# Optimization experiments

Hardware: AMD Instinct MI355X
Metric: run time of the kernel (lower is better)

Reference implementation:

```python
import jax, jax.numpy as jnp
import numpy as np

N = 100000
E = 1600000
DIMS = [256, 192, 128, 64, 3]  # in_features=256, hidden_layer_count=4, last layer -> 3


def setup_inputs() -> dict:
    key = jax.random.key(0)
    ks = jax.random.split(key, 2 + 4 * len(DIMS))
    features = jax.random.normal(ks[0], (N, 256), dtype=jnp.float32)
    # (torch.unique-based normalization implicitly assumes this)
    src = jnp.arange(E, dtype=jnp.int64) % N
    dst = jax.random.randint(ks[1], (E,), 0, N, dtype=jnp.int64)
    edges = jnp.stack([src, dst], axis=1)
    inp = {"features": features, "edges": edges}
    ki = 2
    for li in range(4):
        din, dout = DIMS[li], DIMS[li + 1]
        s = 1.0 / np.sqrt(din)
        inp[f"W0_{li}"] = jax.random.uniform(ks[ki], (din, dout), jnp.float32, -s, s); ki += 1
        inp[f"b0_{li}"] = jax.random.uniform(ks[ki], (dout,), jnp.float32, -s, s); ki += 1
        inp[f"W1_{li}"] = jax.random.uniform(ks[ki], (din, dout), jnp.float32, -s, s); ki += 1
        inp[f"b1_{li}"] = jax.random.uniform(ks[ki], (dout,), jnp.float32, -s, s); ki += 1
    return inp


def _graph_conv_norm(x, edges, deg_inv, W0, b0, W1, b1):
    # pytorch3d GraphConv (undirected): w0(x) + scatter-add of w1(x[neighbor]) over both edge directions,
    # then degree normalization (GraphConvNorm)
    h0 = x @ W0 + b0                       # [N, dout]
    h1 = x @ W1 + b1                       # [N, dout]
    agg = jnp.zeros_like(h0)
    agg = agg.at[edges[:, 0]].add(h1[edges[:, 1]])
    agg = agg.at[edges[:, 1]].add(h1[edges[:, 0]])
    return deg_inv * (h0 + agg)


def reference(features, edges, W0_0, b0_0, W1_0, b1_0, W0_1, b0_1, W1_1, b1_1,
              W0_2, b0_2, W1_2, b1_2, W0_3, b0_3, W1_3, b1_3):
    # degree = occurrence count of each vertex id in edges (== torch.unique(..., return_counts=True)[1])
    deg = jnp.zeros((N,), jnp.float32).at[edges.reshape(-1)].add(1.0)
    deg_inv = (1.0 / deg)[:, None]
    params = [(W0_0, b0_0, W1_0, b1_0), (W0_1, b0_1, W1_1, b1_1), (W0_2, b0_2, W1_2, b1_2)]
    x = features
    for (W0, b0, W1, b1) in params:
        x = jax.nn.relu(_graph_conv_norm(x, edges, deg_inv, W0, b0, W1, b1))
    return _graph_conv_norm(x, edges, deg_inv, W0_3, b0_3, W1_3, b1_3)
```

## Files before the change

kernel.cpp:

```cpp
#include <hip/hip_runtime.h>
#include <hip/hip_fp16.h>

#define NV 100000
#define NE 1600000

#define BM 64
#define BN 64
#define BK 16

#define TBM 128
#define TBN 64
#define TBK 32
#define APAD 40
#define BPAD 40

#define SCAN_B 1024
#define NBLK ((NV + SCAN_B - 1) / SCAN_B)

typedef __attribute__((ext_vector_type(8))) _Float16 f16x8;
typedef __attribute__((ext_vector_type(4))) _Float16 f16x4;
typedef __attribute__((ext_vector_type(2))) _Float16 f16x2;
typedef __attribute__((ext_vector_type(4))) float f32x4;

__global__ void degree_count(const int* __restrict__ ef, int* __restrict__ deg, int n) {
    int i = blockIdx.x * blockDim.x + threadIdx.x;
    if (i < n) atomicAdd(&deg[ef[i]], 1);
}

__global__ __launch_bounds__(SCAN_B) void scan_block(const int* __restrict__ deg,
                                                     int* __restrict__ part,
                                                     int* __restrict__ bsum, int n) {
    __shared__ int tmp[SCAN_B];
    const int tid = threadIdx.x;
    const int gid = blockIdx.x * SCAN_B + tid;
    int v = (gid < n) ? deg[gid] : 0;
    tmp[tid] = v;
    __syncthreads();
    for (int off = 1; off < SCAN_B; off <<= 1) {
        int t = (tid >= off) ? tmp[tid - off] : 0;
        __syncthreads();
        tmp[tid] += t;
        __syncthreads();
    }
    if (gid < n) part[gid] = tmp[tid] - v;
    if (tid == SCAN_B - 1) bsum[blockIdx.x] = tmp[tid];
}

__global__ __launch_bounds__(128) void scan_top(int* __restrict__ bsum, int nb) {
    __shared__ int tmp[128];
    const int tid = threadIdx.x;
    int v = (tid < nb) ? bsum[tid] : 0;
    tmp[tid] = v;
    __syncthreads();
    for (int off = 1; off < 128; off <<= 1) {
        int t = (tid >= off) ? tmp[tid - off] : 0;
        __syncthreads();
        tmp[tid] += t;
        __syncthreads();
    }
    if (tid < nb) bsum[tid] = tmp[tid] - v;
}

__global__ __launch_bounds__(SCAN_B) void finalize_rowptr(int* __restrict__ rowptr,
                                                          const int* __restrict__ bsum,
                                                          const int* __restrict__ deg,
                                                          int* __restrict__ fill,
                                                          float* __restrict__ dinv, int n) {
    const int gid = blockIdx.x * SCAN_B + threadIdx.x;
    if (gid < n) {
        int r = rowptr[gid] + bsum[blockIdx.x];
        rowptr[gid] = r;
        fill[gid] = r;
        dinv[gid] = 1.0f / (float)deg[gid];
    }
    if (gid == 0) rowptr[n] = 2 * NE;
}

__global__ void fill_adj(const int* __restrict__ edges, int* __restrict__ fill,
                         int* __restrict__ adj, int nE) {
    int e = blockIdx.x * blockDim.x + threadIdx.x;
    if (e >= nE) return;
    const int a = edges[2 * e];
    const int b = edges[2 * e + 1];
    int pa = atomicAdd(&fill[a], 1); adj[pa] = b;
    int pb = atomicAdd(&fill[b], 1); adj[pb] = a;
}

template <typename XT>
__global__ __launch_bounds__(256) void gemm_dual_mfma(
    const XT* __restrict__ X,
    const float* __restrict__ W0, const float* __restrict__ b0,
    const float* __restrict__ W1, const float* __restrict__ b1,
    float* __restrict__ C0, _Float16* __restrict__ C1,
    int M, int din, int dout)
{
    __shared__ _Float16 As[TBM * APAD];
    __shared__ _Float16 Bs[2][TBN * BPAD];

    const int tid = threadIdx.x;
    const int bm = blockIdx.x * TBM;
    const int bn = blockIdx.y * TBN;
    const int lane = tid & 63;
    const int wid = tid >> 6;
    const int wm = wid >> 1;
    const int wn = wid & 1;
    const int lr = lane & 15;
    const int lk = lane >> 4;

    f32x4 acc[2][4][2] = {};

    const int bn_n = tid & 63;
    const int bn_kb = (tid >> 6) * 8;

    for (int k0 = 0; k0 < din; k0 += TBK) {
        if constexpr (sizeof(XT) == 4) {
            #pragma unroll
            for (int i = 0; i < 4; ++i) {
                const int idx = tid + i * 256;
                const int row = idx >> 3;
                const int q = idx & 7;
                const int grow = bm + row;
                float4 v = {0.f, 0.f, 0.f, 0.f};
                if (grow < M)
                    v = *reinterpret_cast<const float4*>(&X[(size_t)grow * din + k0 + q * 4]);
                f16x4 h = { (_Float16)v.x, (_Float16)v.y, (_Float16)v.z, (_Float16)v.w };
                *reinterpret_cast<f16x4*>(&As[row * APAD + q * 4]) = h;
            }
        } else {
            #pragma unroll
            for (int i = 0; i < 2; ++i) {
                const int idx = tid + i * 256;
                const int row = idx >> 2;
                const int q = idx & 3;
                const int grow = bm + row;
                f16x8 h = {};
                if (grow < M)
                    h = *reinterpret_cast<const f16x8*>(&X[(size_t)grow * din + k0 + q * 8]);
                *reinterpret_cast<f16x8*>(&As[row * APAD + q * 8]) = h;
            }
        }
        {
            const float* pw0 = &W0[(size_t)(k0 + bn_kb) * dout + bn + bn_n];
            const float* pw1 = &W1[(size_t)(k0 + bn_kb) * dout + bn + bn_n];
            _Float16* d0 = &Bs[0][bn_n * BPAD + bn_kb];
            _Float16* d1 = &Bs[1][bn_n * BPAD + bn_kb];
            #pragma unroll
            for (int i = 0; i < 8; ++i) {
                d0[i] = (_Float16)pw0[(size_t)i * dout];
                d1[i] = (_Float16)pw1[(size_t)i * dout];
            }
        }
        __syncthreads();

        f16x8 a[4], b[2][2];
        #pragma unroll
        for (int mf = 0; mf < 4; ++mf)
            a[mf] = *reinterpret_cast<const f16x8*>(&As[(wm * 64 + mf * 16 + lr) * APAD + lk * 8]);
        #pragma unroll
        for (int o = 0; o < 2; ++o)
            #pragma unroll
            for (int nf = 0; nf < 2; ++nf)
                b[o][nf] = *reinterpret_cast<const f16x8*>(&Bs[o][(wn * 32 + nf * 16 + lr) * BPAD + lk * 8]);

        #pragma unroll
        for (int o = 0; o < 2; ++o)
            #pragma unroll
            for (int mf = 0; mf < 4; ++mf)
                #pragma unroll
                for (int nf = 0; nf < 2; ++nf)
                    acc[o][mf][nf] = __builtin_amdgcn_mfma_f32_16x16x32_f16(
                        a[mf], b[o][nf], acc[o][mf][nf], 0, 0, 0);

        __syncthreads();
    }

    #pragma unroll
    for (int mf = 0; mf < 4; ++mf) {
        #pragma unroll
        for (int reg = 0; reg < 4; ++reg) {
            const int row = bm + wm * 64 + mf * 16 + lk * 4 + reg;
            if (row >= M) continue;
            #pragma unroll
            for (int nf = 0; nf < 2; ++nf) {
                const int c = bn + wn * 32 + nf * 16 + lr;
                C0[(size_t)row * dout + c] = acc[0][mf][nf][reg] + b0[c];
                C1[(size_t)row * dout + c] = (_Float16)(acc[1][mf][nf][reg] + b1[c]);
            }
        }
    }
}

__global__ __launch_bounds__(256) void gemm_dual_bias_f32(
    const _Float16* __restrict__ X,
    const float* __restrict__ W0, const float* __restrict__ b0,
    const float* __restrict__ W1, const float* __restrict__ b1,
    float* __restrict__ C0, float* __restrict__ C1,
    int M, int din, int dout)
{
    __shared__ float As[BM][BK + 1];
    __shared__ float Bs0[BK][BN];
    __shared__ float Bs1[BK][BN];

    const int tid = threadIdx.x;
    const int bm = blockIdx.x * BM;
    const int bn = blockIdx.y * BN;
    const int tx = tid & 15;
    const int ty = tid >> 4;

    const int ar = tid >> 2;
    const int ac = (tid & 3) * 4;
    const int br = tid >> 4;
    const int bc = (tid & 15) * 4;

    float acc0[4][4] = {};
    float acc1[4][4] = {};

    for (int k0 = 0; k0 < din; k0 += BK) {
        {
            const int grow = bm + ar;
            if (grow < M) {
                const f16x4 v = *reinterpret_cast<const f16x4*>(&X[(size_t)grow * din + k0 + ac]);
                As[ar][ac + 0] = (float)v[0]; As[ar][ac + 1] = (float)v[1];
                As[ar][ac + 2] = (float)v[2]; As[ar][ac + 3] = (float)v[3];
            } else {
                As[ar][ac + 0] = 0.f; As[ar][ac + 1] = 0.f;
                As[ar][ac + 2] = 0.f; As[ar][ac + 3] = 0.f;
            }
        }
        {
            const int gk = k0 + br;
            const int gc = bn + bc;
            float4 v0, v1;
            v0.x = (gc + 0 < dout) ? W0[(size_t)gk * dout + gc + 0] : 0.f;
            v0.y = (gc + 1 < dout) ? W0[(size_t)gk * dout + gc + 1] : 0.f;
            v0.z = (gc + 2 < dout) ? W0[(size_t)gk * dout + gc + 2] : 0.f;
            v0.w = (gc + 3 < dout) ? W0[(size_t)gk * dout + gc + 3] : 0.f;
            v1.x = (gc + 0 < dout) ? W1[(size_t)gk * dout + gc + 0] : 0.f;
            v1.y = (gc + 1 < dout) ? W1[(size_t)gk * dout + gc + 1] : 0.f;
            v1.z = (gc + 2 < dout) ? W1[(size_t)gk * dout + gc + 2] : 0.f;
            v1.w = (gc + 3 < dout) ? W1[(size_t)gk * dout + gc + 3] : 0.f;
            *reinterpret_cast<float4*>(&Bs0[br][bc]) = v0;
            *reinterpret_cast<float4*>(&Bs1[br][bc]) = v1;
        }
        __syncthreads();

        #pragma unroll
        for (int kk = 0; kk < BK; ++kk) {
            const float a0 = As[ty * 4 + 0][kk];
            const float a1 = As[ty * 4 + 1][kk];
            const float a2 = As[ty * 4 + 2][kk];
            const float a3 = As[ty * 4 + 3][kk];
            const float4 p = *reinterpret_cast<const float4*>(&Bs0[kk][tx * 4]);
            const float4 q = *reinterpret_cast<const float4*>(&Bs1[kk][tx * 4]);
            acc0[0][0] += a0 * p.x; acc0[0][1] += a0 * p.y; acc0[0][2] += a0 * p.z; acc0[0][3] += a0 * p.w;
            acc0[1][0] += a1 * p.x; acc0[1][1] += a1 * p.y; acc0[1][2] += a1 * p.z; acc0[1][3] += a1 * p.w;
            acc0[2][0] += a2 * p.x; acc0[2][1] += a2 * p.y; acc0[2][2] += a2 * p.z; acc0[2][3] += a2 * p.w;
            acc0[3][0] += a3 * p.x; acc0[3][1] += a3 * p.y; acc0[3][2] += a3 * p.z; acc0[3][3] += a3 * p.w;
            acc1[0][0] += a0 * q.x; acc1[0][1] += a0 * q.y; acc1[0][2] += a0 * q.z; acc1[0][3] += a0 * q.w;
            acc1[1][0] += a1 * q.x; acc1[1][1] += a1 * q.y; acc1[1][2] += a1 * q.z; acc1[1][3] += a1 * q.w;
            acc1[2][0] += a2 * q.x; acc1[2][1] += a2 * q.y; acc1[2][2] += a2 * q.z; acc1[2][3] += a2 * q.w;
            acc1[3][0] += a3 * q.x; acc1[3][1] += a3 * q.y; acc1[3][2] += a3 * q.z; acc1[3][3] += a3 * q.w;
        }
        __syncthreads();
    }

    #pragma unroll
    for (int i = 0; i < 4; ++i) {
        const int row = bm + ty * 4 + i;
        if (row >= M) continue;
        #pragma unroll
        for (int j = 0; j < 4; ++j) {
            const int col = bn + tx * 4 + j;
            if (col < dout) {
                C0[(size_t)row * dout + col] = acc0[i][j] + b0[col];
                C1[(size_t)row * dout + col] = acc1[i][j] + b1[col];
            }
        }
    }
}

__global__ __launch_bounds__(256) void gather_d192_h(
    const float* __restrict__ h0, const __half2* __restrict__ h1,
    const int* __restrict__ rowptr, const int* __restrict__ adj,
    const float* __restrict__ dinv, _Float16* __restrict__ out)
{
    const int v = blockIdx.x * 4 + (threadIdx.x >> 6);
    if (v >= NV) return;
    const int lane = threadIdx.x & 63;
    const int sub = lane >> 5;
    const int cu = (lane & 31) * 3;
    const int s = rowptr[v], e = rowptr[v + 1];

    float2 a0 = {0.f, 0.f}, a1 = {0.f, 0.f}, a2 = {0.f, 0.f};

    int j = s;
    const int jend = s + ((e - s) & ~7);
    for (; j < jend; j += 8) {
        const int u0 = adj[j + 0 + sub];
        const int u1 = adj[j + 2 + sub];
        const int u2 = adj[j + 4 + sub];
        const int u3 = adj[j + 6 + sub];
        const __half2* r0 = h1 + (size_t)u0 * 96 + cu;
        const __half2* r1 = h1 + (size_t)u1 * 96 + cu;
        const __half2* r2 = h1 + (size_t)u2 * 96 + cu;
        const __half2* r3 = h1 + (size_t)u3 * 96 + cu;
        const __half2 x00 = r0[0], x01 = r0[1], x02 = r0[2];
        const __half2 x10 = r1[0], x11 = r1[1], x12 = r1[2];
        const __half2 x20 = r2[0], x21 = r2[1], x22 = r2[2];
        const __half2 x30 = r3[0], x31 = r3[1], x32 = r3[2];
        float2 p;
        p = __half22float2(x00); a0.x += p.x; a0.y += p.y;
        p = __half22float2(x01); a1.x += p.x; a1.y += p.y;
        p = __half22float2(x02); a2.x += p.x; a2.y += p.y;
        p = __half22float2(x10); a0.x += p.x; a0.y += p.y;
        p = __half22float2(x11); a1.x += p.x; a1.y += p.y;
        p = __half22float2(x12); a2.x += p.x; a2.y += p.y;
        p = __half22float2(x20); a0.x += p.x; a0.y += p.y;
        p = __half22float2(x21); a1.x += p.x; a1.y += p.y;
        p = __half22float2(x22); a2.x += p.x; a2.y += p.y;
        p = __half22float2(x30); a0.x += p.x; a0.y += p.y;
        p = __half22float2(x31); a1.x += p.x; a1.y += p.y;
        p = __half22float2(x32); a2.x += p.x; a2.y += p.y;
    }
    for (; j < e; j += 2) {
        const int jj = j + sub;
        if (jj < e) {
            const __half2* r = h1 + (size_t)adj[jj] * 96 + cu;
            float2 p;
            p = __half22float2(r[0]); a0.x += p.x; a0.y += p.y;
            p = __half22float2(r[1]); a1.x += p.x; a1.y += p.y;
            p = __half22float2(r[2]); a2.x += p.x; a2.y += p.y;
        }
    }

    a0.x += __shfl_xor(a0.x, 32); a0.y += __shfl_xor(a0.y, 32);
    a1.x += __shfl_xor(a1.x, 32); a1.y += __shfl_xor(a1.y, 32);
    a2.x += __shfl_xor(a2.x, 32); a2.y += __shfl_xor(a2.y, 32);

    if (sub == 0) {
        const float di = dinv[v];
        const size_t base = (size_t)v * 192 + (size_t)cu * 2;
        f16x2 o0, o1, o2;
        o0[0] = (_Float16)fmaxf((h0[base + 0] + a0.x) * di, 0.f);
        o0[1] = (_Float16)fmaxf((h0[base + 1] + a0.y) * di, 0.f);
        o1[0] = (_Float16)fmaxf((h0[base + 2] + a1.x) * di, 0.f);
        o1[1] = (_Float16)fmaxf((h0[base + 3] + a1.y) * di, 0.f);
        o2[0] = (_Float16)fmaxf((h0[base + 4] + a2.x) * di, 0.f);
        o2[1] = (_Float16)fmaxf((h0[base + 5] + a2.y) * di, 0.f);
        *reinterpret_cast<f16x2*>(out + base + 0) = o0;
        *reinterpret_cast<f16x2*>(out + base + 2) = o1;
        *reinterpret_cast<f16x2*>(out + base + 4) = o2;
    }
}

__global__ __launch_bounds__(256) void gather_d128_h(
    const float* __restrict__ h0, const __half2* __restrict__ h1,
    const int* __restrict__ rowptr, const int* __restrict__ adj,
    const float* __restrict__ dinv, _Float16* __restrict__ out)
{
    const int v = blockIdx.x * 4 + (threadIdx.x >> 6);
    if (v >= NV) return;
    const int lane = threadIdx.x & 63;
    const int sub = lane >> 4;
    const int cu = (lane & 15) * 4;
    const int s = rowptr[v], e = rowptr[v + 1];

    float acc[8] = {};

    int j = s;
    const int jend = s + ((e - s) & ~15);
    for (; j < jend; j += 16) {
        const int u0 = adj[j + 0 + sub];
        const int u1 = adj[j + 4 + sub];
        const int u2 = adj[j + 8 + sub];
        const int u3 = adj[j + 12 + sub];
        const int4 w0 = *reinterpret_cast<const int4*>(h1 + (size_t)u0 * 64 + cu);
        const int4 w1 = *reinterpret_cast<const int4*>(h1 + (size_t)u1 * 64 + cu);
        const int4 w2 = *reinterpret_cast<const int4*>(h1 + (size_t)u2 * 64 + cu);
        const int4 w3 = *reinterpret_cast<const int4*>(h1 + (size_t)u3 * 64 + cu);
        #pragma unroll
        for (int t = 0; t < 4; ++t) {
            const float2 p0 = __half22float2(*(const __half2*)(&(&w0.x)[t]));
            const float2 p1 = __half22float2(*(const __half2*)(&(&w1.x)[t]));
            const float2 p2 = __half22float2(*(const __half2*)(&(&w2.x)[t]));
            const float2 p3 = __half22float2(*(const __half2*)(&(&w3.x)[t]));
            acc[2 * t + 0] += (p0.x + p1.x) + (p2.x + p3.x);
            acc[2 * t + 1] += (p0.y + p1.y) + (p2.y + p3.y);
        }
    }
    for (; j < e; j += 4) {
        const int jj = j + sub;
        if (jj < e) {
            const int4 w0 = *reinterpret_cast<const int4*>(h1 + (size_t)adj[jj] * 64 + cu);
            #pragma unroll
            for (int t = 0; t < 4; ++t) {
                const float2 p = __half22float2(*(const __half2*)(&(&w0.x)[t]));
                acc[2 * t + 0] += p.x;
                acc[2 * t + 1] += p.y;
            }
        }
    }

    #pragma unroll
    for (int t = 0; t < 8; ++t) {
        acc[t] += __shfl_xor(acc[t], 16);
        acc[t] += __shfl_xor(acc[t], 32);
    }

    if (sub == 0) {
        const float di = dinv[v];
        const size_t base = (size_t)v * 128 + (size_t)cu * 2;
        f16x8 o;
        #pragma unroll
        for (int t = 0; t < 8; ++t)
            o[t] = (_Float16)fmaxf((h0[base + t] + acc[t]) * di, 0.f);
        *reinterpret_cast<f16x8*>(out + base) = o;
    }
}

__global__ __launch_bounds__(256) void gather_d64_h(
    const float* __restrict__ h0, const __half2* __restrict__ h1,
    const int* __restrict__ rowptr, const int* __restrict__ adj,
    const float* __restrict__ dinv, _Float16* __restrict__ out)
{
    const int v = blockIdx.x * 4 + (threadIdx.x >> 6);
    if (v >= NV) return;
    const int lane = threadIdx.x & 63;
    const int sub = lane >> 4;
    const int cu = (lane & 15) * 2;
    const int s = rowptr[v], e = rowptr[v + 1];

    float acc[4] = {};

    int j = s;
    const int jend = s + ((e - s) & ~15);
    for (; j < jend; j += 16) {
        const int u0 = adj[j + 0 + sub];
        const int u1 = adj[j + 4 + sub];
        const int u2 = adj[j + 8 + sub];
        const int u3 = adj[j + 12 + sub];
        const int2 w0 = *reinterpret_cast<const int2*>(h1 + (size_t)u0 * 32 + cu);
        const int2 w1 = *reinterpret_cast<const int2*>(h1 + (size_t)u1 * 32 + cu);
        const int2 w2 = *reinterpret_cast<const int2*>(h1 + (size_t)u2 * 32 + cu);
        const int2 w3 = *reinterpret_cast<const int2*>(h1 + (size_t)u3 * 32 + cu);
        #pragma unroll
        for (int t = 0; t < 2; ++t) {
            const float2 p0 = __half22float2(*(const __half2*)(&(&w0.x)[t]));
            const float2 p1 = __half22float2(*(const __half2*)(&(&w1.x)[t]));
            const float2 p2 = __half22float2(*(const __half2*)(&(&w2.x)[t]));
            const float2 p3 = __half22float2(*(const __half2*)(&(&w3.x)[t]));
            acc[2 * t + 0] += (p0.x + p1.x) + (p2.x + p3.x);
            acc[2 * t + 1] += (p0.y + p1.y) + (p2.y + p3.y);
        }
    }
    for (; j < e; j += 4) {
        const int jj = j + sub;
        if (jj < e) {
            const int2 w0 = *reinterpret_cast<const int2*>(h1 + (size_t)adj[jj] * 32 + cu);
            #pragma unroll
            for (int t = 0; t < 2; ++t) {
                const float2 p = __half22float2(*(const __half2*)(&(&w0.x)[t]));
                acc[2 * t + 0] += p.x;
                acc[2 * t + 1] += p.y;
            }
        }
    }

    #pragma unroll
    for (int t = 0; t < 4; ++t) {
        acc[t] += __shfl_xor(acc[t], 16);
        acc[t] += __shfl_xor(acc[t], 32);
    }

    if (sub == 0) {
        const float di = dinv[v];
        const size_t base = (size_t)v * 64 + (size_t)cu * 2;
        f16x4 o;
        #pragma unroll
        for (int t = 0; t < 4; ++t)
            o[t] = (_Float16)fmaxf((h0[base + t] + acc[t]) * di, 0.f);
        *reinterpret_cast<f16x4*>(out + base) = o;
    }
}

__global__ __launch_bounds__(256) void gather_d3(
    const float* __restrict__ h0, const float* __restrict__ h1,
    const int* __restrict__ rowptr, const int* __restrict__ adj,
    const float* __restrict__ dinv, float* __restrict__ out)
{
    const int v = blockIdx.x * 4 + (threadIdx.x >> 6);
    if (v >= NV) return;
    const int lane = threadIdx.x & 63;
    const int s = rowptr[v], e = rowptr[v + 1];
    float a0 = 0.f, a1 = 0.f, a2 = 0.f;
    for (int j = s + lane; j < e; j += 64) {
        const float3 r = *reinterpret_cast<const float3*>(h1 + (size_t)adj[j] * 3);
        a0 += r.x; a1 += r.y; a2 += r.z;
    }
    #pragma unroll
    for (int off = 1; off < 64; off <<= 1) {
        a0 += __shfl_xor(a0, off);
        a1 += __shfl_xor(a1, off);
        a2 += __shfl_xor(a2, off);
    }
    if (lane == 0) {
        const float di = dinv[v];
        const size_t base = (size_t)v * 3;
        out[base + 0] = (h0[base + 0] + a0) * di;
        out[base + 1] = (h0[base + 1] + a1) * di;
        out[base + 2] = (h0[base + 2] + a2) * di;
    }
}

extern "C" void kernel_launch(void* const* d_in, const int* in_sizes, int n_in,
                              void* d_out, int out_size, void* d_ws, size_t ws_size,
                              hipStream_t stream) {
    const float* features = (const float*)d_in[0];
    const int*   edges    = (const int*)d_in[1];

    char* ws = (char*)d_ws;
    size_t off = 0;
    auto alloc = [&](size_t bytes) {
        void* p = ws + off;
        off = (off + bytes + 255) & ~(size_t)255;
        return p;
    };
    int*      deg    = (int*)alloc((size_t)NV * sizeof(int));
    float*    dinv   = (float*)alloc((size_t)NV * sizeof(float));
    int*      rowptr = (int*)alloc((size_t)(NV + 1) * sizeof(int));
    int*      fill   = (int*)alloc((size_t)NV * sizeof(int));
    int*      bsum   = (int*)alloc(256 * sizeof(int));
    int*      adj    = (int*)alloc((size_t)2 * NE * sizeof(int));
    float*    bufC0  = (float*)alloc((size_t)NV * 192 * sizeof(float));
    void*     bufC1  = alloc((size_t)NV * 192 * sizeof(float));
    _Float16* bufX1  = (_Float16*)alloc((size_t)NV * 192 * sizeof(_Float16));
    _Float16* bufX2  = (_Float16*)alloc((size_t)NV * 128 * sizeof(_Float16));

    hipMemsetAsync(deg, 0, (size_t)NV * sizeof(int), stream);
    degree_count<<<(2 * NE + 255) / 256, 256, 0, stream>>>(edges, deg, 2 * NE);
    scan_block<<<NBLK, SCAN_B, 0, stream>>>(deg, rowptr, bsum, NV);
    scan_top<<<1, 128, 0, stream>>>(bsum, NBLK);
    finalize_rowptr<<<NBLK, SCAN_B, 0, stream>>>(rowptr, bsum, deg, fill, dinv, NV);
    fill_adj<<<(NE + 255) / 256, 256, 0, stream>>>(edges, fill, adj, NE);

    const int gatherGrid = (NV + 3) / 4;
    const int dims[5] = {256, 192, 128, 64, 3};
    _Float16* Xh[4] = { nullptr, bufX1, bufX2, bufX1 };
    _Float16* Xout[3] = { bufX1, bufX2, bufX1 };

    for (int li = 0; li < 4; ++li) {
        const int din  = dims[li];
        const int dout = dims[li + 1];
        const float* W0 = (const float*)d_in[2 + li * 4 + 0];
        const float* b0 = (const float*)d_in[2 + li * 4 + 1];
        const float* W1 = (const float*)d_in[2 + li * 4 + 2];
        const float* b1 = (const float*)d_in[2 + li * 4 + 3];

        if (li == 0) {
            dim3 grid((NV + TBM - 1) / TBM, dout / TBN);
            gemm_dual_mfma<float><<<grid, 256, 0, stream>>>(features, W0, b0, W1, b1,
                                                            bufC0, (_Float16*)bufC1, NV, din, dout);
        } else if (li < 3) {
            dim3 grid((NV + TBM - 1) / TBM, dout / TBN);
            gemm_dual_mfma<_Float16><<<grid, 256, 0, stream>>>(Xh[li], W0, b0, W1, b1,
                                                               bufC0, (_Float16*)bufC1, NV, din, dout);
        } else {
            dim3 grid((NV + BM - 1) / BM, (dout + BN - 1) / BN);
            gemm_dual_bias_f32<<<grid, 256, 0, stream>>>(Xh[li], W0, b0, W1, b1,
                                                         bufC0, (float*)bufC1, NV, din, dout);
        }

        if (li == 0)
            gather_d192_h<<<gatherGrid, 256, 0, stream>>>(bufC0, (const __half2*)bufC1,
                                                          rowptr, adj, dinv, Xout[0]);
        else if (li == 1)
            gather_d128_h<<<gatherGrid, 256, 0, stream>>>(bufC0, (const __half2*)bufC1,
                                                          rowptr, adj, dinv, Xout[1]);
        else if (li == 2)
            gather_d64_h<<<gatherGrid, 256, 0, stream>>>(bufC0, (const __half2*)bufC1,
                                                         rowptr, adj, dinv, Xout[2]);
        else
            gather_d3<<<gatherGrid, 256, 0, stream>>>(bufC0, (const float*)bufC1,
                                                      rowptr, adj, dinv, (float*)d_out);
    }
}
```

Measured before the change: 786.2 us.

## Load full-K row panel once per block and store h0 in fp16

The dual GEMM now loads a 96-row panel of X covering the whole input dimension into shared memory once. It then loops over all output column tiles inside one block, so X is no longer re-read for each column tile through grid.y. The self-term output h0 is also stored as fp16 instead of fp32, and the gather kernels read it with vector loads, which halves that intermediate's traffic. The costs are larger shared memory per block (lower occupancy), fewer blocks in the grid, and extra fp16 rounding on h0.

```diff
diff --git a/kernel.cpp b/kernel.cpp
--- a/kernel.cpp
+++ b/kernel.cpp
@@ -7,12 +7,6 @@
 #define BM 64
 #define BN 64
 #define BK 16
-
-#define TBM 128
-#define TBN 64
-#define TBK 32
-#define APAD 40
-#define BPAD 40
 
 #define SCAN_B 1024
 #define NBLK ((NV + SCAN_B - 1) / SCAN_B)
@@ -86,20 +80,22 @@
     int pb = atomicAdd(&fill[b], 1); adj[pb] = a;
 }
 
-template <typename XT>
-__global__ __launch_bounds__(256) void gemm_dual_mfma(
+template <typename XT, int DIN, int NT>
+__global__ __launch_bounds__(256) void gemm_dual_panel(
     const XT* __restrict__ X,
     const float* __restrict__ W0, const float* __restrict__ b0,
     const float* __restrict__ W1, const float* __restrict__ b1,
-    float* __restrict__ C0, _Float16* __restrict__ C1,
-    int M, int din, int dout)
+    _Float16* __restrict__ C0, _Float16* __restrict__ C1, int M)
 {
-    __shared__ _Float16 As[TBM * APAD];
-    __shared__ _Float16 Bs[2][TBN * BPAD];
+    constexpr int DOUT = NT * 64;
+    constexpr int AST = DIN + 12;
+    constexpr int BST = 44;
+
+    __shared__ _Float16 As[96 * AST];
+    __shared__ _Float16 Bs[2][64 * BST];
 
     const int tid = threadIdx.x;
-    const int bm = blockIdx.x * TBM;
-    const int bn = blockIdx.y * TBN;
+    const int bm = blockIdx.x * 96;
     const int lane = tid & 63;
     const int wid = tid >> 6;
     const int wm = wid >> 1;
@@ -107,84 +103,88 @@
     const int lr = lane & 15;
     const int lk = lane >> 4;
 
-    f32x4 acc[2][4][2] = {};
-
-    const int bn_n = tid & 63;
-    const int bn_kb = (tid >> 6) * 8;
-
-    for (int k0 = 0; k0 < din; k0 += TBK) {
-        if constexpr (sizeof(XT) == 4) {
+    if constexpr (sizeof(XT) == 4) {
+        constexpr int QPR = DIN / 4;
+        for (int idx = tid; idx < 96 * QPR; idx += 256) {
+            const int row = idx / QPR, q = idx % QPR;
+            const int grow = bm + row;
+            float4 v = {0.f, 0.f, 0.f, 0.f};
+            if (grow < M)
+                v = *reinterpret_cast<const float4*>(&X[(size_t)grow * DIN + q * 4]);
+            f16x4 h = { (_Float16)v.x, (_Float16)v.y, (_Float16)v.z, (_Float16)v.w };
+            *reinterpret_cast<f16x4*>(&As[row * AST + q * 4]) = h;
+        }
+    } else {
+        constexpr int QPR = DIN / 8;
+        for (int idx = tid; idx < 96 * QPR; idx += 256) {
+            const int row = idx / QPR, q = idx % QPR;
+            const int grow = bm + row;
+            f16x8 h = {};
+            if (grow < M)
+                h = *reinterpret_cast<const f16x8*>(&X[(size_t)grow * DIN + q * 8]);
+            *reinterpret_cast<f16x8*>(&As[row * AST + q * 8]) = h;
+        }
+    }
+    __syncthreads();
+
+    const int ccol = tid & 63;
+    const int kb = (tid >> 6) * 8;
+
+    #pragma unroll
+    for (int nt = 0; nt < NT; ++nt) {
+        const int bn = nt * 64;
+        f32x4 acc[2][3][2] = {};
+
+        for (int k0 = 0; k0 < DIN; k0 += 32) {
+            {
+                const float* pw0 = &W0[(size_t)(k0 + kb) * DOUT + bn + ccol];
+                const float* pw1 = &W1[(size_t)(k0 + kb) * DOUT + bn + ccol];
+                _Float16* d0 = &Bs[0][ccol * BST + kb];
+                _Float16* d1 = &Bs[1][ccol * BST + kb];
+                #pragma unroll
+                for (int i = 0; i < 8; ++i) {
+                    d0[i] = (_Float16)pw0[(size_t)i * DOUT];
+                    d1[i] = (_Float16)pw1[(size_t)i * DOUT];
+                }
+            }
+            __syncthreads();
+
+            f16x8 a[3], b[2][2];
             #pragma unroll
-            for (int i = 0; i < 4; ++i) {
-                const int idx = tid + i * 256;
-                const int row = idx >> 3;
-                const int q = idx & 7;
-                const int grow = bm + row;
-                float4 v = {0.f, 0.f, 0.f, 0.f};
-                if (grow < M)
-                    v = *reinterpret_cast<const float4*>(&X[(size_t)grow * din + k0 + q * 4]);
-                f16x4 h = { (_Float16)v.x, (_Float16)v.y, (_Float16)v.z, (_Float16)v.w };
-                *reinterpret_cast<f16x4*>(&As[row * APAD + q * 4]) = h;
-            }
-        } else {
+            for (int mf = 0; mf < 3; ++mf)
+                a[mf] = *reinterpret_cast<const f16x8*>(
+                    &As[(wm * 48 + mf * 16 + lr) * AST + k0 + lk * 8]);
             #pragma unroll
-            for (int i = 0; i < 2; ++i) {
-                const int idx = tid + i * 256;
-                const int row = idx >> 2;
-                const int q = idx & 3;
-                const int grow = bm + row;
-                f16x8 h = {};
-                if (grow < M)
-                    h = *reinterpret_cast<const f16x8*>(&X[(size_t)grow * din + k0 + q * 8]);
-                *reinterpret_cast<f16x8*>(&As[row * APAD + q * 8]) = h;
-            }
-        }
-        {
-            const float* pw0 = &W0[(size_t)(k0 + bn_kb) * dout + bn + bn_n];
-            const float* pw1 = &W1[(size_t)(k0 + bn_kb) * dout + bn + bn_n];
-            _Float16* d0 = &Bs[0][bn_n * BPAD + bn_kb];
-            _Float16* d1 = &Bs[1][bn_n * BPAD + bn_kb];
-            #pragma unroll
-            for (int i = 0; i < 8; ++i) {
-                d0[i] = (_Float16)pw0[(size_t)i * dout];
-                d1[i] = (_Float16)pw1[(size_t)i * dout];
-            }
-        }
-        __syncthreads();
-
-        f16x8 a[4], b[2][2];
-        #pragma unroll
-        for (int mf = 0; mf < 4; ++mf)
-            a[mf] = *reinterpret_cast<const f16x8*>(&As[(wm * 64 + mf * 16 + lr) * APAD + lk * 8]);
-        #pragma unroll
-        for (int o = 0; o < 2; ++o)
-            #pragma unroll
-            for (int nf = 0; nf < 2; ++nf)
-                b[o][nf] = *reinterpret_cast<const f16x8*>(&Bs[o][(wn * 32 + nf * 16 + lr) * BPAD + lk * 8]);
-
-        #pragma unroll
-        for (int o = 0; o < 2; ++o)
-            #pragma unroll
-            for (int mf = 0; mf < 4; ++mf)
+            for (int o = 0; o < 2; ++o)
                 #pragma unroll
                 for (int nf = 0; nf < 2; ++nf)
-                    acc[o][mf][nf] = __builtin_amdgcn_mfma_f32_16x16x32_f16(
-                        a[mf], b[o][nf], acc[o][mf][nf], 0, 0, 0);
-
-        __syncthreads();
-    }
-
-    #pragma unroll
-    for (int mf = 0; mf < 4; ++mf) {
-        #pragma unroll
-        for (int reg = 0; reg < 4; ++reg) {
-            const int row = bm + wm * 64 + mf * 16 + lk * 4 + reg;
-            if (row >= M) continue;
+                    b[o][nf] = *reinterpret_cast<const f16x8*>(
+                        &Bs[o][(wn * 32 + nf * 16 + lr) * BST + lk * 8]);
+
             #pragma unroll
-            for (int nf = 0; nf < 2; ++nf) {
-                const int c = bn + wn * 32 + nf * 16 + lr;
-                C0[(size_t)row * dout + c] = acc[0][mf][nf][reg] + b0[c];
-                C1[(size_t)row * dout + c] = (_Float16)(acc[1][mf][nf][reg] + b1[c]);
+            for (int o = 0; o < 2; ++o)
+                #pragma unroll
+                for (int mf = 0; mf < 3; ++mf)
+                    #pragma unroll
+                    for (int nf = 0; nf < 2; ++nf)
+                        acc[o][mf][nf] = __builtin_amdgcn_mfma_f32_16x16x32_f16(
+                            a[mf], b[o][nf], acc[o][mf][nf], 0, 0, 0);
+
+            __syncthreads();
+        }
+
+        #pragma unroll
+        for (int mf = 0; mf < 3; ++mf) {
+            #pragma unroll
+            for (int reg = 0; reg < 4; ++reg) {
+                const int row = bm + wm * 48 + mf * 16 + lk * 4 + reg;
+                if (row >= M) continue;
+                #pragma unroll
+                for (int nf = 0; nf < 2; ++nf) {
+                    const int c = bn + wn * 32 + nf * 16 + lr;
+                    C0[(size_t)row * DOUT + c] = (_Float16)(acc[0][mf][nf][reg] + b0[c]);
+                    C1[(size_t)row * DOUT + c] = (_Float16)(acc[1][mf][nf][reg] + b1[c]);
+                }
             }
         }
     }
@@ -280,7 +280,7 @@
 }
 
 __global__ __launch_bounds__(256) void gather_d192_h(
-    const float* __restrict__ h0, const __half2* __restrict__ h1,
+    const _Float16* __restrict__ h0, const __half2* __restrict__ h1,
     const int* __restrict__ rowptr, const int* __restrict__ adj,
     const float* __restrict__ dinv, _Float16* __restrict__ out)
 {
@@ -340,13 +340,16 @@
     if (sub == 0) {
         const float di = dinv[v];
         const size_t base = (size_t)v * 192 + (size_t)cu * 2;
+        const f16x2 z0 = *reinterpret_cast<const f16x2*>(h0 + base + 0);
+        const f16x2 z1 = *reinterpret_cast<const f16x2*>(h0 + base + 2);
+        const f16x2 z2 = *reinterpret_cast<const f16x2*>(h0 + base + 4);
         f16x2 o0, o1, o2;
-        o0[0] = (_Float16)fmaxf((h0[base + 0] + a0.x) * di, 0.f);
-        o0[1] = (_Float16)fmaxf((h0[base + 1] + a0.y) * di, 0.f);
-        o1[0] = (_Float16)fmaxf((h0[base + 2] + a1.x) * di, 0.f);
-        o1[1] = (_Float16)fmaxf((h0[base + 3] + a1.y) * di, 0.f);
-        o2[0] = (_Float16)fmaxf((h0[base + 4] + a2.x) * di, 0.f);
-        o2[1] = (_Float16)fmaxf((h0[base + 5] + a2.y) * di, 0.f);
+        o0[0] = (_Float16)fmaxf(((float)z0[0] + a0.x) * di, 0.f);
+        o0[1] = (_Float16)fmaxf(((float)z0[1] + a0.y) * di, 0.f);
+        o1[0] = (_Float16)fmaxf(((float)z1[0] + a1.x) * di, 0.f);
+        o1[1] = (_Float16)fmaxf(((float)z1[1] + a1.y) * di, 0.f);
+        o2[0] = (_Float16)fmaxf(((float)z2[0] + a2.x) * di, 0.f);
+        o2[1] = (_Float16)fmaxf(((float)z2[1] + a2.y) * di, 0.f);
         *reinterpret_cast<f16x2*>(out + base + 0) = o0;
         *reinterpret_cast<f16x2*>(out + base + 2) = o1;
         *reinterpret_cast<f16x2*>(out + base + 4) = o2;
@@ -354,7 +357,7 @@
 }
 
 __global__ __launch_bounds__(256) void gather_d128_h(
-    const float* __restrict__ h0, const __half2* __restrict__ h1,
+    const _Float16* __restrict__ h0, const __half2* __restrict__ h1,
     const int* __restrict__ rowptr, const int* __restrict__ adj,
     const float* __restrict__ dinv, _Float16* __restrict__ out)
 {
@@ -410,16 +413,17 @@
     if (sub == 0) {
         const float di = dinv[v];
         const size_t base = (size_t)v * 128 + (size_t)cu * 2;
+        const f16x8 z = *reinterpret_cast<const f16x8*>(h0 + base);
         f16x8 o;
         #pragma unroll
         for (int t = 0; t < 8; ++t)
-            o[t] = (_Float16)fmaxf((h0[base + t] + acc[t]) * di, 0.f);
+            o[t] = (_Float16)fmaxf(((float)z[t] + acc[t]) * di, 0.f);
         *reinterpret_cast<f16x8*>(out + base) = o;
     }
 }
 
 __global__ __launch_bounds__(256) void gather_d64_h(
-    const float* __restrict__ h0, const __half2* __restrict__ h1,
+    const _Float16* __restrict__ h0, const __half2* __restrict__ h1,
     const int* __restrict__ rowptr, const int* __restrict__ adj,
     const float* __restrict__ dinv, _Float16* __restrict__ out)
 {
@@ -475,10 +479,11 @@
     if (sub == 0) {
         const float di = dinv[v];
         const size_t base = (size_t)v * 64 + (size_t)cu * 2;
+        const f16x4 z = *reinterpret_cast<const f16x4*>(h0 + base);
         f16x4 o;
         #pragma unroll
         for (int t = 0; t < 4; ++t)
-            o[t] = (_Float16)fmaxf((h0[base + t] + acc[t]) * di, 0.f);
+            o[t] = (_Float16)fmaxf(((float)z[t] + acc[t]) * di, 0.f);
         *reinterpret_cast<f16x4*>(out + base) = o;
     }
 }
@@ -531,10 +536,12 @@
     int*      fill   = (int*)alloc((size_t)NV * sizeof(int));
     int*      bsum   = (int*)alloc(256 * sizeof(int));
     int*      adj    = (int*)alloc((size_t)2 * NE * sizeof(int));
-    float*    bufC0  = (float*)alloc((size_t)NV * 192 * sizeof(float));
-    void*     bufC1  = alloc((size_t)NV * 192 * sizeof(float));
+    _Float16* hC0    = (_Float16*)alloc((size_t)NV * 192 * sizeof(_Float16));
+    _Float16* hC1    = (_Float16*)alloc((size_t)NV * 192 * sizeof(_Float16));
     _Float16* bufX1  = (_Float16*)alloc((size_t)NV * 192 * sizeof(_Float16));
     _Float16* bufX2  = (_Float16*)alloc((size_t)NV * 128 * sizeof(_Float16));
+    float*    c0f    = (float*)alloc((size_t)NV * 3 * sizeof(float));
+    float*    c1f    = (float*)alloc((size_t)NV * 3 * sizeof(float));
 
     hipMemsetAsync(deg, 0, (size_t)NV * sizeof(int), stream);
     degree_count<<<(2 * NE + 255) / 256, 256, 0, stream>>>(edges, deg, 2 * NE);
@@ -544,43 +551,39 @@
     fill_adj<<<(NE + 255) / 256, 256, 0, stream>>>(edges, fill, adj, NE);
 
     const int gatherGrid = (NV + 3) / 4;
-    const int dims[5] = {256, 192, 128, 64, 3};
-    _Float16* Xh[4] = { nullptr, bufX1, bufX2, bufX1 };
-    _Float16* Xout[3] = { bufX1, bufX2, bufX1 };
-
-    for (int li = 0; li < 4; ++li) {
-        const int din  = dims[li];
-        const int dout = dims[li + 1];
-        const float* W0 = (const float*)d_in[2 + li * 4 + 0];
-        const float* b0 = (const float*)d_in[2 + li * 4 + 1];
-        const float* W1 = (const float*)d_in[2 + li * 4 + 2];
-        const float* b1 = (const float*)d_in[2 + li * 4 + 3];
-
-        if (li == 0) {
-            dim3 grid((NV + TBM - 1) / TBM, dout / TBN);
-            gemm_dual_mfma<float><<<grid, 256, 0, stream>>>(features, W0, b0, W1, b1,
-                                                            bufC0, (_Float16*)bufC1, NV, din, dout);
-        } else if (li < 3) {
-            dim3 grid((NV + TBM - 1) / TBM, dout / TBN);
-            gemm_dual_mfma<_Float16><<<grid, 256, 0, stream>>>(Xh[li], W0, b0, W1, b1,
-                                                               bufC0, (_Float16*)bufC1, NV, din, dout);
-        } else {
-            dim3 grid((NV + BM - 1) / BM, (dout + BN - 1) / BN);
-            gemm_dual_bias_f32<<<grid, 256, 0, stream>>>(Xh[li], W0, b0, W1, b1,
-                                                         bufC0, (float*)bufC1, NV, din, dout);
-        }
-
-        if (li == 0)
-            gather_d192_h<<<gatherGrid, 256, 0, stream>>>(bufC0, (const __half2*)bufC1,
-                                                          rowptr, adj, dinv, Xout[0]);
-        else if (li == 1)
-            gather_d128_h<<<gatherGrid, 256, 0, stream>>>(bufC0, (const __half2*)bufC1,
-                                                          rowptr, adj, dinv, Xout[1]);
-        else if (li == 2)
-            gather_d64_h<<<gatherGrid, 256, 0, stream>>>(bufC0, (const __half2*)bufC1,
-                                                         rowptr, adj, dinv, Xout[2]);
-        else
-            gather_d3<<<gatherGrid, 256, 0, stream>>>(bufC0, (const float*)bufC1,
-                                                      rowptr, adj, dinv, (float*)d_out);
-    }
-}
+    const int panelGrid = (NV + 95) / 96;
+
+    gemm_dual_panel<float, 256, 3><<<panelGrid, 256, 0, stream>>>(
+        features,
+        (const float*)d_in[2], (const float*)d_in[3],
+        (const float*)d_in[4], (const float*)d_in[5],
+        hC0, hC1, NV);
+    gather_d192_h<<<gatherGrid, 256, 0, stream>>>(hC0, (const __half2*)hC1,
+                                                  rowptr, adj, dinv, bufX1);
+
+    gemm_dual_panel<_Float16, 192, 2><<<panelGrid, 256, 0, stream>>>(
+        bufX1,
+        (const float*)d_in[6], (const float*)d_in[7],
+        (const float*)d_in[8], (const float*)d_in[9],
+        hC0, hC1, NV);
+    gather_d128_h<<<gatherGrid, 256, 0, stream>>>(hC0, (const __half2*)hC1,
+                                                  rowptr, adj, dinv, bufX2);
+
+    gemm_dual_panel<_Float16, 128, 1><<<panelGrid, 256, 0, stream>>>(
+        bufX2,
+        (const float*)d_in[10], (const float*)d_in[11],
+        (const float*)d_in[12], (const float*)d_in[13],
+        hC0, hC1, NV);
+    gather_d64_h<<<gatherGrid, 256, 0, stream>>>(hC0, (const __half2*)hC1,
+                                                 rowptr, adj, dinv, bufX1);
+
+    {
+        dim3 grid((NV + BM - 1) / BM, 1);
+        gemm_dual_bias_f32<<<grid, 256, 0, stream>>>(
+            bufX1,
+            (const float*)d_in[14], (const float*)d_in[15],
+            (const float*)d_in[16], (const float*)d_in[17],
+            c0f, c1f, NV, 64, 3);
+        gather_d3<<<gatherGrid, 256, 0, stream>>>(c0f, c1f, rowptr, adj, dinv, (float*)d_out);
+    }
+}
```

New measurement: 761.3 us. 1.03x faster.
